# Kernel optimization log

Measured on AMD Instinct MI355X. Metric: run time of the kernel, lower is better.

The kernel has to match this reference:

```python
import jax, jax.numpy as jnp
import numpy as np
from jax import lax

T = 5        # unrolled ISTA iterations (module default)
LAM = 0.1    # soft-threshold level (module default)
B, L, K = 4096, 4096, 128


def _conv1d_same(x, k):
    """TF-style SAME cross-correlation. x: [B, L], k: [K] -> [B, L]."""
    Kw = k.shape[0]
    pad_left = (Kw - 1) // 2
    pad_right = Kw - 1 - pad_left
    out = lax.conv_general_dilated(
        x[:, None, :],            # [B, 1, L]
        k[None, None, :],         # [O=1, I=1, K]
        window_strides=(1,),
        padding=[(pad_left, pad_right)],
        dimension_numbers=("NCH", "OIH", "NCH"),
    )
    return out[:, 0, :]


def setup_inputs() -> dict:
    key = jax.random.key(0)
    k1, k2 = jax.random.split(key)
    y = jax.random.normal(k1, (B, L), dtype=jnp.float32)
    thz_pulse = jax.random.normal(k2, (K,), dtype=jnp.float32)  # learned pulse (trainable)
    step_size = jnp.full((1,), 0.1, dtype=jnp.float32)          # learned step (trainable)
    return {"y": y, "thz_pulse": thz_pulse, "step_size": step_size}


def reference(y, thz_pulse, step_size):
    x = jnp.zeros_like(y)
    h = thz_pulse           # matched-filter kernel
    h_rev = thz_pulse[::-1] # time-reversed kernel (adjoint / correlation)
    s = step_size[0]
    for _ in range(T):
        conv_out = _conv1d_same(y, h)           # H y
        residual = y - conv_out                 # y - H y
        update = _conv1d_same(residual, h_rev)  # H^T residual
        x = x + s * update                      # gradient step
        x = jnp.sign(x) * jax.nn.relu(jnp.abs(x) - LAM)  # soft-threshold
    return x
```

## Files before the change

kernel.cpp:

```cpp
#include <hip/hip_runtime.h>


typedef __bf16 bf16;
typedef __bf16 bf16x4 __attribute__((ext_vector_type(4)));
typedef __bf16 bf16x8 __attribute__((ext_vector_type(8)));
typedef float f32x4 __attribute__((ext_vector_type(4)));

#define LAM 0.1f
#define WS_AG 0
#define WS_ZERO 80
#define WS_A1 8192
#define WS_A2 12288
#define PYE 360
#define PRE 216

__global__ __launch_bounds__(256) void ista_prep(const float* __restrict__ h,
                                                 bf16* __restrict__ ws) {
  __shared__ float hs[256];
  __shared__ float acp[256];
  __shared__ bf16 gp[384];
  const int tid = threadIdx.x;
  hs[tid] = (tid < 128) ? h[tid] : 0.f;
  gp[tid] = (bf16)0.f;
  if (tid < 128) gp[256 + tid] = (bf16)0.f;
  __syncthreads();
  const int tau = tid & 127;
  {
    const int m0 = (tid >> 7) * 64;
    float p0 = 0.f, p1 = 0.f, p2 = 0.f, p3 = 0.f;
    for (int m = m0; m < m0 + 64; m += 4) {
      p0 += hs[m] * hs[m + tau];     p1 += hs[m + 1] * hs[m + 1 + tau];
      p2 += hs[m + 2] * hs[m + 2 + tau]; p3 += hs[m + 3] * hs[m + 3 + tau];
    }
    acp[tid] = (p0 + p1) + (p2 + p3);
  }
  __syncthreads();
  if (tid < 128) {
    float ac = acp[tid] + acp[tid + 128];
    float g1 = (tau <= 63) ? hs[63 - tau] : 0.f;
    gp[145 + tau] = (bf16)(g1 - ac);
    if (tau > 0) {
      float g2 = (tau <= 64) ? hs[63 + tau] : 0.f;
      gp[145 - tau] = (bf16)(g2 - ac);
    }
  }
  __syncthreads();
  for (int i = tid; i < 1024; i += 256) {
    const int l = i >> 4, dd = i & 15;
    if (dd < 9) {
      const int o = 144 + (l >> 4) * 8 - (l & 15) + (dd - 4) * 32;
      bf16x8 a;
#pragma unroll
      for (int j = 0; j < 8; ++j) a[j] = gp[o + j];
      *reinterpret_cast<bf16x8*>(ws + WS_AG + l * 128 + dd * 8) = a;
    }
  }
  if (tid < 8) ws[WS_ZERO + tid] = (bf16)0.f;
  for (int i = tid; i < 512; i += 256) {
    const int l = i >> 3, dd = i & 7;
    if (dd < 5) {
      const int o = 127 + (l >> 4) * 8 - (l & 15) + (dd - 2) * 32;
      bf16x8 a1, a2;
#pragma unroll
      for (int j = 0; j < 8; ++j) {
        int p = o + j;
        int i1 = p - 64;
        a1[j] = ((unsigned)i1 < 128u) ? (bf16)hs[i1] : (bf16)0.f;
        int i2 = 191 - p;
        a2[j] = ((unsigned)i2 < 128u) ? (bf16)(-hs[i2]) : (bf16)0.f;
      }
      *reinterpret_cast<bf16x8*>(ws + WS_A1 + l * 64 + dd * 8) = a1;
      *reinterpret_cast<bf16x8*>(ws + WS_A2 + l * 64 + dd * 8) = a2;
    }
  }
}

__device__ __forceinline__ bf16x8 ldfrag(const float* __restrict__ rowb,
                                         int col) {
  const int X = col & 1023;
  float4 v0 = *reinterpret_cast<const float4*>(rowb + X);
  float4 v1 = *reinterpret_cast<const float4*>(rowb + X + 4);
  bf16x8 b;
  b[0] = (bf16)v0.x; b[1] = (bf16)v0.y; b[2] = (bf16)v0.z; b[3] = (bf16)v0.w;
  b[4] = (bf16)v1.x; b[5] = (bf16)v1.y; b[6] = (bf16)v1.z; b[7] = (bf16)v1.w;
  return b;
}

__global__ __launch_bounds__(256) void ista_fused(
    const float* __restrict__ y, const bf16* __restrict__ ws,
    const float* __restrict__ step, float* __restrict__ out) {
  __shared__ __align__(16) char smem[65536];
  const int tid = threadIdx.x;
  const int lane = tid & 63;
  const int li = lane & 15;
  const int quad = tid >> 4 & 3;
  const int wave = tid >> 6;
  const int bid = blockIdx.x;
  const float s = step[0];

  if (bid < 512) {
    const int b0 = (bid & 255) * 16;
    const int cb = (bid >> 8) * 2048;

    bf16x8 AG[9];
#pragma unroll
    for (int dd = 0; dd < 9; ++dd)
      AG[dd] = *reinterpret_cast<const bf16x8*>(ws + WS_AG + lane * 128 + dd * 8);

    const float* zsrc = reinterpret_cast<const float*>(ws + WS_ZERO);
    const int r0 = wave * 4;
    auto issue_seg = [&](int m) {
      const int base = cb + 128 * m;
      const bool oob = (base < 0) | (base >= 4096) | (m > 17);
      const int slotB = ((128 * m) & 1023) << 2;
#pragma unroll
      for (int t = 0; t < 8; ++t) {
        const int r = r0 + (t >> 1);
        const int q = t & 1;
        const float* src =
            oob ? zsrc : (y + (size_t)(b0 + r) * 4096 + base + 64 * q + lane);
        char* dst = smem + r * 4096 + slotB + q * 256;
        __builtin_amdgcn_global_load_lds(
            (const __attribute__((address_space(1))) void*)src,
            (__attribute__((address_space(3))) void*)dst, 4, 0, 0);
      }
    };

#pragma unroll
    for (int m = -1; m <= 4; ++m) issue_seg(m);

    const int qo = quad << 3;
    const float* rowb = reinterpret_cast<const float*>(smem) + li * 1024;
    float* orow = out + (size_t)(b0 + li) * 4096 + cb + (quad << 2);
    bf16x8 B[9];

#pragma unroll
    for (int k = 0; k < 16; ++k) {
      asm volatile("s_waitcnt vmcnt(16)" ::: "memory");
      __builtin_amdgcn_s_barrier();
      __builtin_amdgcn_sched_barrier(0);
      issue_seg(k + 5);
      if (k == 0) {
#pragma unroll
        for (int dd = 0; dd < 9; ++dd)
          B[dd] = ldfrag(rowb, 16 * wave + (dd - 4) * 32 + qo);
      }
#pragma unroll
      for (int j = 0; j < 2; ++j) {
        const int tc = 128 * k + 64 * j + 16 * wave;
        bf16x8 n0 = ldfrag(rowb, tc + 160 + qo);
        bf16x8 n1 = ldfrag(rowb, tc + 192 + qo);
        f32x4 acc0 = {0.f, 0.f, 0.f, 0.f};
        f32x4 acc1 = {0.f, 0.f, 0.f, 0.f};
        acc0 = __builtin_amdgcn_mfma_f32_16x16x32_bf16(AG[0], B[0], acc0, 0, 0, 0);
        acc1 = __builtin_amdgcn_mfma_f32_16x16x32_bf16(AG[1], B[1], acc1, 0, 0, 0);
        acc0 = __builtin_amdgcn_mfma_f32_16x16x32_bf16(AG[2], B[2], acc0, 0, 0, 0);
        acc1 = __builtin_amdgcn_mfma_f32_16x16x32_bf16(AG[3], B[3], acc1, 0, 0, 0);
        acc0 = __builtin_amdgcn_mfma_f32_16x16x32_bf16(AG[4], B[4], acc0, 0, 0, 0);
        acc1 = __builtin_amdgcn_mfma_f32_16x16x32_bf16(AG[5], B[5], acc1, 0, 0, 0);
        acc0 = __builtin_amdgcn_mfma_f32_16x16x32_bf16(AG[6], B[6], acc0, 0, 0, 0);
        acc1 = __builtin_amdgcn_mfma_f32_16x16x32_bf16(AG[7], B[7], acc1, 0, 0, 0);
        acc0 = __builtin_amdgcn_mfma_f32_16x16x32_bf16(AG[8], B[8], acc0, 0, 0, 0);
        const int tabs = cb + tc;
        if (tabs >= 64 && tabs < 4032) {
          float4 xv;
#pragma unroll
          for (int e = 0; e < 4; ++e) {
            float su = s * (acc0[e] + acc1[e]);
            float ax = fabsf(su) - LAM;
            ax = ax > 0.f ? ax : 0.f;
            (&xv.x)[e] = 5.f * copysignf(ax, su);
          }
          *reinterpret_cast<float4*>(orow + tc) = xv;
        }
        B[0] = B[2]; B[1] = B[3]; B[2] = B[4]; B[3] = B[5]; B[4] = B[6];
        B[5] = B[7]; B[6] = B[8]; B[7] = n0; B[8] = n1;
      }
    }
  } else {
    const int eid = bid - 512;
    const int chunk0 = (eid & 1) ? (4096 - 64) : 0;
    const int b0 = (eid >> 1) * 16;
    bf16* ys = reinterpret_cast<bf16*>(smem);
    bf16* rs = ys + 16 * PYE;
    const int wv = wave;

    bf16x8 A1[5], A2[5];
#pragma unroll
    for (int dd = 0; dd < 5; ++dd) {
      A1[dd] = *reinterpret_cast<const bf16x8*>(ws + WS_A1 + lane * 64 + dd * 8);
      A2[dd] = *reinterpret_cast<const bf16x8*>(ws + WS_A2 + lane * 64 + dd * 8);
    }

    {
      const int rr = tid >> 4;
      const int t = tid & 15;
      const float* yrow = y + (size_t)(b0 + rr) * 4096;
      bf16* dst = ys + rr * PYE;
#pragma unroll
      for (int k = 0; k < 6; ++k) {
        int s4 = t + 16 * k;
        if (s4 < 88) {
          int l = chunk0 - 128 + s4 * 4;
          float4 v;
          if (l >= 0 && l <= 4096 - 4) {
            v = *reinterpret_cast<const float4*>(yrow + l);
          } else {
            v.x = ((unsigned)(l + 0) < 4096u) ? yrow[l + 0] : 0.f;
            v.y = ((unsigned)(l + 1) < 4096u) ? yrow[l + 1] : 0.f;
            v.z = ((unsigned)(l + 2) < 4096u) ? yrow[l + 2] : 0.f;
            v.w = ((unsigned)(l + 3) < 4096u) ? yrow[l + 3] : 0.f;
          }
          bf16x4 bv;
          bv[0] = (bf16)v.x; bv[1] = (bf16)v.y; bv[2] = (bf16)v.z; bv[3] = (bf16)v.w;
          *reinterpret_cast<bf16x4*>(dst + s4 * 4) = bv;
        }
      }
    }
    __syncthreads();

    for (int t = wv; t < 13; t += 4) {
      const int i0 = -64 + 16 * t;
      f32x4 acc;
      {
        bf16x4 yv = *reinterpret_cast<const bf16x4*>(
            ys + li * PYE + (i0 + 128) + quad * 4);
        acc[0] = -(float)yv[0]; acc[1] = -(float)yv[1];
        acc[2] = -(float)yv[2]; acc[3] = -(float)yv[3];
      }
#pragma unroll
      for (int dd = 0; dd < 5; ++dd) {
        bf16x8 b = *reinterpret_cast<const bf16x8*>(
            ys + li * PYE + (i0 + (dd - 2) * 32 + 128) + quad * 8);
        acc = __builtin_amdgcn_mfma_f32_16x16x32_bf16(A1[dd], b, acc, 0, 0, 0);
      }
      bf16x4 rv;
#pragma unroll
      for (int e = 0; e < 4; ++e) {
        int g = chunk0 + i0 + quad * 4 + e;
        float v = ((unsigned)g < 4096u) ? acc[e] : 0.f;
        rv[e] = (bf16)v;
      }
      *reinterpret_cast<bf16x4*>(rs + li * PRE + (i0 + 64) + quad * 4) = rv;
    }
    __syncthreads();

    {
      const int i0 = 16 * wv;
      f32x4 acc = {0.f, 0.f, 0.f, 0.f};
#pragma unroll
      for (int dd = 0; dd < 5; ++dd) {
        bf16x8 b = *reinterpret_cast<const bf16x8*>(
            rs + li * PRE + (i0 + (dd - 2) * 32 + 64) + quad * 8);
        acc = __builtin_amdgcn_mfma_f32_16x16x32_bf16(A2[dd], b, acc, 0, 0, 0);
      }
      float4 xv;
#pragma unroll
      for (int e = 0; e < 4; ++e) {
        float su = s * acc[e];
        float ax = fabsf(su) - LAM;
        ax = ax > 0.f ? ax : 0.f;
        (&xv.x)[e] = 5.f * copysignf(ax, su);
      }
      *reinterpret_cast<float4*>(
          out + (size_t)(b0 + li) * 4096 + chunk0 + i0 + quad * 4) = xv;
    }
  }
}

extern "C" void kernel_launch(void* const* d_in, const int* in_sizes, int n_in,
                              void* d_out, int out_size, void* d_ws,
                              size_t ws_size, hipStream_t stream) {
  const float* y = (const float*)d_in[0];
  const float* h = (const float*)d_in[1];
  const float* s = (const float*)d_in[2];
  float* out = (float*)d_out;
  bf16* ws = (bf16*)d_ws;
  ista_prep<<<dim3(1), dim3(256), 0, stream>>>(h, ws);
  ista_fused<<<dim3(512 + 512), dim3(256), 0, stream>>>(y, ws, s, out);
}
```

Before: 152.9 us.

## Shrink LDS ring to six segments with padded rows and move barrier

Replaces the 1024-column per-row LDS ring buffer (64 KB) with a 768-column ring using a padded row stride of 772 floats (~49 KB). The prefetch depth drops from 6 to 5 segments, and the wait-and-barrier moves to the end of each iteration with running wrapped offsets. The aim is to let more blocks fit per CU and to reduce LDS bank conflicts through row padding. The cost is one less segment of prefetch lookahead and modulo index arithmetic.

```diff
diff --git a/kernel.cpp b/kernel.cpp
--- a/kernel.cpp
+++ b/kernel.cpp
@@ -7,6 +7,9 @@
 typedef float f32x4 __attribute__((ext_vector_type(4)));
 
 #define LAM 0.1f
+#define RPDW 772
+#define RCOLS 768
+#define LDSB (16 * RPDW * 4)
 #define WS_AG 0
 #define WS_ZERO 80
 #define WS_A1 8192
@@ -75,9 +78,8 @@
   }
 }
 
-__device__ __forceinline__ bf16x8 ldfrag(const float* __restrict__ rowb,
-                                         int col) {
-  const int X = col & 1023;
+__device__ __forceinline__ bf16x8 ldfragX(const float* __restrict__ rowb,
+                                          int X) {
   float4 v0 = *reinterpret_cast<const float4*>(rowb + X);
   float4 v1 = *reinterpret_cast<const float4*>(rowb + X + 4);
   bf16x8 b;
@@ -89,11 +91,11 @@
 __global__ __launch_bounds__(256) void ista_fused(
     const float* __restrict__ y, const bf16* __restrict__ ws,
     const float* __restrict__ step, float* __restrict__ out) {
-  __shared__ __align__(16) char smem[65536];
+  __shared__ __align__(16) char smem[LDSB];
   const int tid = threadIdx.x;
   const int lane = tid & 63;
   const int li = lane & 15;
-  const int quad = tid >> 4 & 3;
+  const int quad = (tid >> 4) & 3;
   const int wave = tid >> 6;
   const int bid = blockIdx.x;
   const float s = step[0];
@@ -111,15 +113,15 @@
     const int r0 = wave * 4;
     auto issue_seg = [&](int m) {
       const int base = cb + 128 * m;
-      const bool oob = (base < 0) | (base >= 4096) | (m > 17);
-      const int slotB = ((128 * m) & 1023) << 2;
+      const bool oob = ((unsigned)base >= 4096u);
+      const int slotB = (((m + 6) % 6) * 128) << 2;
 #pragma unroll
       for (int t = 0; t < 8; ++t) {
         const int r = r0 + (t >> 1);
         const int q = t & 1;
         const float* src =
             oob ? zsrc : (y + (size_t)(b0 + r) * 4096 + base + 64 * q + lane);
-        char* dst = smem + r * 4096 + slotB + q * 256;
+        char* dst = smem + r * (RPDW * 4) + slotB + q * 256;
         __builtin_amdgcn_global_load_lds(
             (const __attribute__((address_space(1))) void*)src,
             (__attribute__((address_space(3))) void*)dst, 4, 0, 0);
@@ -127,29 +129,30 @@
     };
 
 #pragma unroll
-    for (int m = -1; m <= 4; ++m) issue_seg(m);
+    for (int m = -1; m <= 3; ++m) issue_seg(m);
+    asm volatile("s_waitcnt vmcnt(8)" ::: "memory");
+    __builtin_amdgcn_s_barrier();
+    __builtin_amdgcn_sched_barrier(0);
 
     const int qo = quad << 3;
-    const float* rowb = reinterpret_cast<const float*>(smem) + li * 1024;
+    const float* rowb = reinterpret_cast<const float*>(smem) + li * RPDW;
     float* orow = out + (size_t)(b0 + li) * 4096 + cb + (quad << 2);
+
     bf16x8 B[9];
-
-#pragma unroll
+#pragma unroll
+    for (int dd = 0; dd < 9; ++dd) {
+      int col = 16 * wave + (dd - 4) * 32 + qo;
+      B[dd] = ldfragX(rowb, (col + RCOLS) % RCOLS);
+    }
+    int o0 = 16 * wave + 160 + qo;
+    int o1 = o0 + 32;
+
     for (int k = 0; k < 16; ++k) {
-      asm volatile("s_waitcnt vmcnt(16)" ::: "memory");
-      __builtin_amdgcn_s_barrier();
-      __builtin_amdgcn_sched_barrier(0);
-      issue_seg(k + 5);
-      if (k == 0) {
-#pragma unroll
-        for (int dd = 0; dd < 9; ++dd)
-          B[dd] = ldfrag(rowb, 16 * wave + (dd - 4) * 32 + qo);
-      }
+      issue_seg(k + 4);
 #pragma unroll
       for (int j = 0; j < 2; ++j) {
-        const int tc = 128 * k + 64 * j + 16 * wave;
-        bf16x8 n0 = ldfrag(rowb, tc + 160 + qo);
-        bf16x8 n1 = ldfrag(rowb, tc + 192 + qo);
+        bf16x8 n0 = ldfragX(rowb, o0);
+        bf16x8 n1 = ldfragX(rowb, o1);
         f32x4 acc0 = {0.f, 0.f, 0.f, 0.f};
         f32x4 acc1 = {0.f, 0.f, 0.f, 0.f};
         acc0 = __builtin_amdgcn_mfma_f32_16x16x32_bf16(AG[0], B[0], acc0, 0, 0, 0);
@@ -161,6 +164,7 @@
         acc0 = __builtin_amdgcn_mfma_f32_16x16x32_bf16(AG[6], B[6], acc0, 0, 0, 0);
         acc1 = __builtin_amdgcn_mfma_f32_16x16x32_bf16(AG[7], B[7], acc1, 0, 0, 0);
         acc0 = __builtin_amdgcn_mfma_f32_16x16x32_bf16(AG[8], B[8], acc0, 0, 0, 0);
+        const int tc = 128 * k + 64 * j + 16 * wave;
         const int tabs = cb + tc;
         if (tabs >= 64 && tabs < 4032) {
           float4 xv;
@@ -175,7 +179,12 @@
         }
         B[0] = B[2]; B[1] = B[3]; B[2] = B[4]; B[3] = B[5]; B[4] = B[6];
         B[5] = B[7]; B[6] = B[8]; B[7] = n0; B[8] = n1;
-      }
+        o0 += 64; if (o0 >= RCOLS) o0 -= RCOLS;
+        o1 += 64; if (o1 >= RCOLS) o1 -= RCOLS;
+      }
+      asm volatile("s_waitcnt vmcnt(8)" ::: "memory");
+      __builtin_amdgcn_s_barrier();
+      __builtin_amdgcn_sched_barrier(0);
     }
   } else {
     const int eid = bid - 512;
```

Result: faster. 134.6 us (-12.0%).
